# Performance work log

Measured on AMD Instinct MI355X. Metric: run time of the kernel, lower is better.

The kernel has to match this reference:

```python
import jax, jax.numpy as jnp
import numpy as np

B, T, NODES, DEG = 16, 50, 62, 8
IN, C, H, NC, K = 64, 128, 256, 3, 5
G = B * T            # num_graphs
N = G * NODES        # total nodes
E = G * NODES * DEG  # total edges (before self loops)


def setup_inputs() -> dict:
    key = jax.random.key(0)
    ks = jax.random.split(key, 12)
    # random within-graph edges, PyG-batched with node offsets
    rng = np.random.RandomState(0)
    src = rng.randint(0, NODES, size=(G, NODES * DEG))
    dst = rng.randint(0, NODES, size=(G, NODES * DEG))
    off = (np.arange(G) * NODES)[:, None]
    edge_index = jnp.asarray(np.stack([(src + off).ravel(), (dst + off).ravel()]), dtype=jnp.int32)

    def glorot(k, shape, fan_in):
        return jax.random.normal(k, shape, jnp.float32) / np.sqrt(fan_in)

    return {
        "x": jax.random.normal(ks[0], (N, IN), jnp.float32),
        "edge_index": edge_index,
        "edge_attr": jax.random.normal(ks[1], (E, 1), jnp.float32),
        "W_l": glorot(ks[2], (IN, C), IN), "b_l": jnp.zeros((C,), jnp.float32),
        "W_r": glorot(ks[3], (IN, C), IN), "b_r": jnp.zeros((C,), jnp.float32),
        "W_e": glorot(ks[4], (1, C), 1),
        "att": glorot(ks[5], (C,), C),
        "bias_out": jnp.zeros((C,), jnp.float32),
        "W_ih": glorot(ks[6], (3 * H, C), C), "W_hh": glorot(ks[7], (3 * H, H), H),
        "b_ih": jnp.zeros((3 * H,), jnp.float32), "b_hh": jnp.zeros((3 * H,), jnp.float32),
        "W1": glorot(ks[8], (H, H // 2), H), "b1": jnp.zeros((H // 2,), jnp.float32),
        "W2": glorot(ks[9], (H // 2, NC), H // 2), "b2": jnp.zeros((NC,), jnp.float32),
    }


def _forward(x, edge_index, edge_attr, W_l, b_l, W_r, b_r, W_e, att, bias_out,
             W_ih, W_hh, b_ih, b_hh, W1, b1, W2, b2):
    n = x.shape[0]
    src, dst = edge_index[0], edge_index[1]

    # --- GATv2Conv: add self loops with edge_attr fill_value='mean' (PyG default) ---
    sum_attr = jax.ops.segment_sum(edge_attr, dst, num_segments=n)
    cnt = jax.ops.segment_sum(jnp.ones_like(dst, jnp.float32), dst, num_segments=n)
    loop_attr = sum_attr / jnp.clip(cnt, 1.0)[:, None]
    ar = jnp.arange(n, dtype=src.dtype)
    src2 = jnp.concatenate([src, ar])
    dst2 = jnp.concatenate([dst, ar])
    ea = jnp.concatenate([edge_attr, loop_attr], axis=0)

    xl = x @ W_l + b_l          # source-side transform
    xr = x @ W_r + b_r          # target-side transform
    ee = ea @ W_e               # edge embedding (lin_edge, bias=False)

    m = xl[src2] + xr[dst2] + ee                # [E2, C]
    e = jax.nn.leaky_relu(m, 0.2) @ att         # [E2]
    # scatter-softmax over incoming edges per target node (self loops => no empty segs)
    emax = jax.ops.segment_max(e, dst2, num_segments=n)
    ez = jnp.exp(e - emax[dst2])
    den = jax.ops.segment_sum(ez, dst2, num_segments=n)
    alpha = ez / den[dst2]                      # [E2]
    h_sp = jax.ops.segment_sum(alpha[:, None] * xl[src2], dst2, num_segments=n) + bias_out

    # --- mean pool per graph (uniform graph size => reshape) ---
    g = h_sp.reshape(G, NODES, C).mean(axis=1).reshape(B, T, C)

    # --- GRU (PyTorch gate order r, z, n) ---
    def step(h, xt):
        gx = xt @ W_ih.T + b_ih
        gh = h @ W_hh.T + b_hh
        xr_, xz, xn = jnp.split(gx, 3, axis=-1)
        hr, hz, hn = jnp.split(gh, 3, axis=-1)
        r = jax.nn.sigmoid(xr_ + hr)
        z = jax.nn.sigmoid(xz + hz)
        nn_ = jnp.tanh(xn + r * hn)
        h2 = (1.0 - z) * nn_ + z * h
        return h2, h2

    h0 = jnp.zeros((B, H), g.dtype)
    _, hs = jax.lax.scan(step, h0, jnp.swapaxes(g, 0, 1))  # [T,B,H]
    gru_out = jnp.swapaxes(hs, 0, 1)                       # [B,T,H]

    # --- classifier (dropout inactive at eval) ---
    scores = jax.nn.relu(gru_out @ W1 + b1) @ W2 + b2      # [B,T,NC]

    # --- top-k over time per class, then mean over k ---
    vals, idx = jax.lax.top_k(jnp.swapaxes(scores, 1, 2), K)  # [B,NC,K]
    return vals.mean(axis=-1), jnp.swapaxes(idx, 1, 2)        # [B,NC], [B,K,NC]


def reference(x, edge_index, edge_attr, W_l, b_l, W_r, b_r, W_e, att, bias_out,
              W_ih, W_hh, b_ih, b_hh, W1, b1, W2, b2):
    return _forward(x, edge_index, edge_attr, W_l, b_l, W_r, b_r, W_e, att, bias_out,
                    W_ih, W_hh, b_ih, b_hh, W1, b1, W2, b2)
```

## Files before the change

kernel.cpp:

```cpp
#include <hip/hip_runtime.h>
#include <math.h>

#define NNODES 62
#define NDEG 8
#define NGRAPH 800
#define NB 16
#define NT 50
#define NIN 64
#define NCH 128
#define NH 256
#define NCLS 3
#define NTOPK 5
#define NSL 8
#define EPG (NNODES*NDEG)
#define E2G (EPG + NNODES)
#define NTOTAL (NGRAPH*NNODES)
#define ETOTAL (NGRAPH*EPG)

__launch_bounds__(256, 2)
__global__ void k_xrl(const float* __restrict__ x,
                      const float* __restrict__ W_r, const float* __restrict__ b_r,
                      const float* __restrict__ W_l, const float* __restrict__ b_l,
                      float* __restrict__ xr, float* __restrict__ xl) {
    __shared__ __align__(16) float x_s[64 * NIN];
    __shared__ __align__(16) float wr_s[NIN * NCH];
    __shared__ __align__(16) float wl_s[NIN * NCH];
    const int blk = blockIdx.x;
    const int tid = threadIdx.x;
    const int base_v = blk * 64;

    {
        const float4* src = reinterpret_cast<const float4*>(x + (size_t)base_v * NIN);
        float4* dst = reinterpret_cast<float4*>(x_s);
        for (int i = tid; i < 64 * NIN / 4; i += 256) dst[i] = src[i];
        const float4* sr = reinterpret_cast<const float4*>(W_r);
        const float4* sl = reinterpret_cast<const float4*>(W_l);
        float4* dr = reinterpret_cast<float4*>(wr_s);
        float4* dl = reinterpret_cast<float4*>(wl_s);
        for (int i = tid; i < NIN * NCH / 4; i += 256) { dr[i] = sr[i]; dl[i] = sl[i]; }
    }
    __syncthreads();

    const int c4 = (tid & 31) * 4;
    const int ng = tid >> 5;
    float4 aR[8], aL[8];
    float4 br4 = *reinterpret_cast<const float4*>(b_r + c4);
    float4 bl4 = *reinterpret_cast<const float4*>(b_l + c4);
    #pragma unroll
    for (int j = 0; j < 8; ++j) { aR[j] = br4; aL[j] = bl4; }

    const float* xs = x_s + (ng * 8) * NIN;
    for (int k4 = 0; k4 < NIN; k4 += 4) {
        float4 xv[8];
        #pragma unroll
        for (int j = 0; j < 8; ++j)
            xv[j] = *reinterpret_cast<const float4*>(&xs[j * NIN + k4]);
        #pragma unroll
        for (int kk = 0; kk < 4; ++kk) {
            float4 wr = *reinterpret_cast<const float4*>(&wr_s[(k4 + kk) * NCH + c4]);
            float4 wl = *reinterpret_cast<const float4*>(&wl_s[(k4 + kk) * NCH + c4]);
            #pragma unroll
            for (int j = 0; j < 8; ++j) {
                float xk = (kk == 0) ? xv[j].x : (kk == 1) ? xv[j].y
                         : (kk == 2) ? xv[j].z : xv[j].w;
                aR[j].x += xk * wr.x; aR[j].y += xk * wr.y;
                aR[j].z += xk * wr.z; aR[j].w += xk * wr.w;
                aL[j].x += xk * wl.x; aL[j].y += xk * wl.y;
                aL[j].z += xk * wl.z; aL[j].w += xk * wl.w;
            }
        }
    }
    #pragma unroll
    for (int j = 0; j < 8; ++j) {
        int v = base_v + ng * 8 + j;
        *reinterpret_cast<float4*>(xr + (size_t)v * NCH + c4) = aR[j];
        *reinterpret_cast<float4*>(xl + (size_t)v * NCH + c4) = aL[j];
    }
}

__global__ void k_transpose(const float* __restrict__ src, float* __restrict__ dst,
                            int rows, int cols) {
    int idx = blockIdx.x * blockDim.x + threadIdx.x;
    if (idx >= rows * cols) return;
    int r = idx / cols;
    int c = idx - r * cols;
    dst[c * rows + r] = src[idx];
}

__launch_bounds__(256, 4)
__global__ void k_gat(const int* __restrict__ ei, const float* __restrict__ eattr,
                      const float* __restrict__ W_e, const float* __restrict__ att,
                      const float* __restrict__ bias_out,
                      const float* __restrict__ xr_all, const float* __restrict__ xl_all,
                      float* __restrict__ g_all) {
    __shared__ __align__(16) float xl_s[NNODES * NCH];
    __shared__ unsigned short csr_src[E2G];
    __shared__ float csr_attr[E2G];
    __shared__ float csr_e[E2G];
    __shared__ unsigned short off_s[NNODES + 2];
    __shared__ unsigned cur_s[NNODES];
    __shared__ unsigned cnt_s[NNODES];
    __shared__ float asum_s[NNODES];
    __shared__ float la_s[NNODES];
    __shared__ float gacc_s[4 * NCH];

    const int g = blockIdx.x;
    const int tid = threadIdx.x;
    const int base_e = g * EPG;
    const int base_n = g * NNODES;

    for (int v = tid; v < NNODES; v += 256) { asum_s[v] = 0.f; cnt_s[v] = 0u; cur_s[v] = 0u; }
    {
        const float4* src = reinterpret_cast<const float4*>(xl_all + (size_t)base_n * NCH);
        float4* dst = reinterpret_cast<float4*>(xl_s);
        for (int i = tid; i < NNODES * NCH / 4; i += 256) dst[i] = src[i];
    }
    int s0 = -1, d0 = 0, s1 = -1, d1 = 0;
    float a0 = 0.f, a1 = 0.f;
    {
        int j0 = tid * 2, j1 = tid * 2 + 1;
        if (j0 < EPG) { s0 = ei[base_e + j0] - base_n; d0 = ei[ETOTAL + base_e + j0] - base_n; a0 = eattr[base_e + j0]; }
        if (j1 < EPG) { s1 = ei[base_e + j1] - base_n; d1 = ei[ETOTAL + base_e + j1] - base_n; a1 = eattr[base_e + j1]; }
    }
    __syncthreads();

    if (s0 >= 0) { atomicAdd(&cnt_s[d0], 1u); atomicAdd(&asum_s[d0], a0); }
    if (s1 >= 0) { atomicAdd(&cnt_s[d1], 1u); atomicAdd(&asum_s[d1], a1); }
    __syncthreads();

    if (tid < 64) {
        unsigned val = (tid < NNODES) ? (cnt_s[tid] + 1u) : 0u;
        unsigned xsc = val;
        #pragma unroll
        for (int dlt = 1; dlt < 64; dlt <<= 1) {
            unsigned o = __shfl_up(xsc, dlt, 64);
            if (tid >= dlt) xsc += o;
        }
        if (tid < NNODES) {
            off_s[tid] = (unsigned short)(xsc - val);
            la_s[tid] = asum_s[tid] / fmaxf((float)cnt_s[tid], 1.f);
        }
        if (tid == NNODES - 1) off_s[NNODES] = (unsigned short)xsc;
    }
    __syncthreads();

    if (s0 >= 0) { int sl = off_s[d0] + (int)atomicAdd(&cur_s[d0], 1u); csr_src[sl] = (unsigned short)s0; csr_attr[sl] = a0; }
    if (s1 >= 0) { int sl = off_s[d1] + (int)atomicAdd(&cur_s[d1], 1u); csr_src[sl] = (unsigned short)s1; csr_attr[sl] = a1; }
    if (tid < NNODES) { int sl = off_s[tid + 1] - 1; csr_src[sl] = (unsigned short)tid; csr_attr[sl] = la_s[tid]; }
    __syncthreads();

    const int wave = tid >> 6;
    const int lane = tid & 63;
    const int sub = lane & 15;
    const int gslot = wave * 4 + (lane >> 4);
    const int cb = sub * 8;

    float we0[8], at0[8];
    #pragma unroll
    for (int i = 0; i < 8; ++i) { we0[i] = W_e[cb + i]; at0[i] = att[cb + i]; }

    float acc[8];
    #pragma unroll
    for (int i = 0; i < 8; ++i) acc[i] = 0.f;

    for (int v = gslot; v < NNODES; v += 16) {
        const float* xrp = xr_all + (size_t)(base_n + v) * NCH + cb;
        float4 xr0 = *reinterpret_cast<const float4*>(xrp);
        float4 xr1 = *reinterpret_cast<const float4*>(xrp + 4);
        const int lo = off_s[v], hi = off_s[v + 1];
        float m = -INFINITY, ssum = 0.f;
        for (int sl = lo; sl < hi; ++sl) {
            int src = csr_src[sl];
            float a = csr_attr[sl];
            float4 x0 = *reinterpret_cast<const float4*>(&xl_s[src * NCH + cb]);
            float4 x1 = *reinterpret_cast<const float4*>(&xl_s[src * NCH + cb + 4]);
            float m0, t = 0.f;
            m0 = x0.x + xr0.x + a * we0[0]; t += (m0 >= 0.f ? m0 : 0.2f * m0) * at0[0];
            m0 = x0.y + xr0.y + a * we0[1]; t += (m0 >= 0.f ? m0 : 0.2f * m0) * at0[1];
            m0 = x0.z + xr0.z + a * we0[2]; t += (m0 >= 0.f ? m0 : 0.2f * m0) * at0[2];
            m0 = x0.w + xr0.w + a * we0[3]; t += (m0 >= 0.f ? m0 : 0.2f * m0) * at0[3];
            m0 = x1.x + xr1.x + a * we0[4]; t += (m0 >= 0.f ? m0 : 0.2f * m0) * at0[4];
            m0 = x1.y + xr1.y + a * we0[5]; t += (m0 >= 0.f ? m0 : 0.2f * m0) * at0[5];
            m0 = x1.z + xr1.z + a * we0[6]; t += (m0 >= 0.f ? m0 : 0.2f * m0) * at0[6];
            m0 = x1.w + xr1.w + a * we0[7]; t += (m0 >= 0.f ? m0 : 0.2f * m0) * at0[7];
            t += __shfl_xor(t, 1, 64);
            t += __shfl_xor(t, 2, 64);
            t += __shfl_xor(t, 4, 64);
            t += __shfl_xor(t, 8, 64);
            if (sub == 0) csr_e[sl] = t;
            float mn = fmaxf(m, t);
            ssum = ssum * __expf(m - mn) + __expf(t - mn);
            m = mn;
        }
        float inv = 1.f / ssum;
        for (int sl = lo; sl < hi; ++sl) {
            int src = csr_src[sl];
            float al = __expf(csr_e[sl] - m) * inv;
            float4 x0 = *reinterpret_cast<const float4*>(&xl_s[src * NCH + cb]);
            float4 x1 = *reinterpret_cast<const float4*>(&xl_s[src * NCH + cb + 4]);
            acc[0] += al * x0.x; acc[1] += al * x0.y;
            acc[2] += al * x0.z; acc[3] += al * x0.w;
            acc[4] += al * x1.x; acc[5] += al * x1.y;
            acc[6] += al * x1.z; acc[7] += al * x1.w;
        }
    }
    #pragma unroll
    for (int i = 0; i < 8; ++i) {
        acc[i] += __shfl_xor(acc[i], 16, 64);
        acc[i] += __shfl_xor(acc[i], 32, 64);
    }
    if ((lane >> 4) == 0) {
        *reinterpret_cast<float4*>(&gacc_s[wave * NCH + cb]) =
            make_float4(acc[0], acc[1], acc[2], acc[3]);
        *reinterpret_cast<float4*>(&gacc_s[wave * NCH + cb + 4]) =
            make_float4(acc[4], acc[5], acc[6], acc[7]);
    }
    __syncthreads();

    for (int c = tid; c < NCH; c += 256) {
        float v = (gacc_s[c] + gacc_s[NCH + c] + gacc_s[2 * NCH + c] + gacc_s[3 * NCH + c])
                      * (1.f / NNODES) + bias_out[c];
        g_all[(size_t)g * NCH + c] = v;
    }
}

__global__ void k_gx(const float* __restrict__ g_all, const float* __restrict__ W_ihT,
                     const float* __restrict__ b_ih, const float* __restrict__ b_hh,
                     float* __restrict__ gx_all, unsigned long long* __restrict__ h_pub) {
    if (blockIdx.x < 32)
        h_pub[(size_t)blockIdx.x * 256 + threadIdx.x] = 0ull;
    int idx = blockIdx.x * blockDim.x + threadIdx.x;
    if (idx >= NGRAPH * 3 * NH) return;
    int gi = idx / (3 * NH);
    int o = idx - gi * (3 * NH);
    float acc = b_ih[o] + (o < 2 * NH ? b_hh[o] : 0.f);
    const float* grow = g_all + (size_t)gi * NCH;
    for (int c = 0; c < NCH; ++c) acc += grow[c] * W_ihT[c * (3 * NH) + o];
    gx_all[idx] = acc;
}

__launch_bounds__(256)
__global__ void k_gru(const float* __restrict__ gx_all, const float* __restrict__ W_hh,
                      const float* __restrict__ b_hh, float* __restrict__ h_all,
                      unsigned long long* __restrict__ h_pub) {
    __shared__ __align__(16) float h_s[NH];
    __shared__ float gh_s[96];
    __shared__ float gx_s[2][96];

    const int bid = blockIdx.x;
    const int b = bid >> 3;
    const int s = bid & 7;
    const int tid = threadIdx.x;
    const int wv = tid >> 6;
    const int g = tid >> 1;
    const int l = tid & 1;

    float4 Wv[32];
    if (tid < 192) {
        int row = (g / 32) * NH + 32 * s + (g & 31);
        const float* wr = W_hh + (size_t)row * NH + 128 * l;
        #pragma unroll
        for (int j = 0; j < 32; ++j) Wv[j] = *reinterpret_cast<const float4*>(wr + 4 * j);
    }
    const float bhn = (tid < 32) ? b_hh[2 * NH + 32 * s + tid] : 0.f;
    const int own_lo = 32 * s, own_hi = own_lo + 32;

    for (int i = tid; i < NH; i += 256) h_s[i] = 0.f;
    if (wv == 3) {
        int i = tid - 192;
        int o = (i < 32) ? (32 * s + i) : (NH + 32 * s + (i - 32));
        gx_s[0][i] = gx_all[(size_t)(b * NT) * (3 * NH) + o];
        if (i < 32) gx_s[0][i + 64] = gx_all[(size_t)(b * NT) * (3 * NH) + 2 * NH + 32 * s + i];
    }
    __syncthreads();

    for (int t = 0; t < NT; ++t) {
        const int par = (t + 1) & 1;
        if (wv == 3) {
            int i = tid - 192;
            if (t + 1 < NT) {
                size_t base = (size_t)(b * NT + t + 1) * (3 * NH);
                int o = (i < 32) ? (32 * s + i) : (NH + 32 * s + (i - 32));
                gx_s[par][i] = gx_all[base + o];
                if (i < 32) gx_s[par][i + 64] = gx_all[base + 2 * NH + 32 * s + i];
            }
        } else {
            float a0 = 0.f, a1 = 0.f, a2 = 0.f, a3 = 0.f;
            #pragma unroll
            for (int j = 0; j < 32; ++j) {
                float4 hv = *reinterpret_cast<const float4*>(&h_s[128 * l + 4 * j]);
                float4 w = Wv[j];
                a0 += w.x * hv.x; a1 += w.y * hv.y; a2 += w.z * hv.z; a3 += w.w * hv.w;
            }
            float acc = (a0 + a1) + (a2 + a3);
            acc += __shfl_xor(acc, 1, 64);
            if (l == 0) gh_s[g] = acc;
        }
        __syncthreads();

        if (tid < 32) {
            const float* gx = gx_s[t & 1];
            float r = 1.f / (1.f + expf(-(gx[tid] + gh_s[tid])));
            float z = 1.f / (1.f + expf(-(gx[32 + tid] + gh_s[32 + tid])));
            float n = tanhf(gx[64 + tid] + r * (gh_s[64 + tid] + bhn));
            int o = own_lo + tid;
            float hv = (1.f - z) * n + z * h_s[o];
            h_all[(size_t)(b * NT + t) * NH + o] = hv;
            unsigned long long w = ((unsigned long long)(unsigned)(t + 1) << 32)
                                 | (unsigned long long)__float_as_uint(hv);
            __hip_atomic_store(&h_pub[((size_t)b * 2 + par) * NH + o], w,
                               __ATOMIC_RELAXED, __HIP_MEMORY_SCOPE_AGENT);
            h_s[o] = hv;
        }
        if (tid < own_lo || tid >= own_hi) {
            const unsigned long long* p = &h_pub[((size_t)b * 2 + par) * NH + tid];
            unsigned long long w;
            const unsigned target = (unsigned)(t + 1);
            while ((unsigned)((w = __hip_atomic_load(p, __ATOMIC_RELAXED,
                                                     __HIP_MEMORY_SCOPE_AGENT)) >> 32) != target)
                ;
            h_s[tid] = __uint_as_float((unsigned)w);
        }
        __syncthreads();
    }
}

__launch_bounds__(128)
__global__ void k_cls(const float* __restrict__ h_all,
                      const float* __restrict__ W1, const float* __restrict__ b1,
                      const float* __restrict__ W2, const float* __restrict__ b2,
                      float* __restrict__ sc_all) {
    __shared__ float h_s[NH];
    __shared__ float s1_s[NH / 2];
    const int bt = blockIdx.x;
    const int tid = threadIdx.x;
    h_s[tid] = h_all[(size_t)bt * NH + tid];
    h_s[tid + 128] = h_all[(size_t)bt * NH + tid + 128];
    __syncthreads();
    float acc = b1[tid];
    #pragma unroll 8
    for (int k = 0; k < NH; ++k) acc += h_s[k] * W1[k * (NH / 2) + tid];
    s1_s[tid] = fmaxf(acc, 0.f);
    __syncthreads();
    if (tid < NCLS) {
        float a = b2[tid];
        for (int k = 0; k < NH / 2; ++k) a += s1_s[k] * W2[k * NCLS + tid];
        sc_all[bt * NCLS + tid] = a;
    }
}

__global__ void k_topk(const float* __restrict__ sc_all, float* __restrict__ out) {
    int tid = threadIdx.x;
    if (tid >= NB * NCLS) return;
    int b = tid / NCLS;
    int c = tid - b * NCLS;
    float vals[NT];
    for (int t = 0; t < NT; ++t) vals[t] = sc_all[(b * NT + t) * NCLS + c];
    float sum = 0.f;
    for (int k = 0; k < NTOPK; ++k) {
        float best = -INFINITY; int bi = 0;
        for (int t = 0; t < NT; ++t) {
            if (vals[t] > best) { best = vals[t]; bi = t; }
        }
        vals[bi] = -INFINITY;
        sum += best;
        out[NB * NCLS + b * (NTOPK * NCLS) + k * NCLS + c] = (float)bi;
    }
    out[b * NCLS + c] = sum * (1.f / NTOPK);
}

extern "C" void kernel_launch(void* const* d_in, const int* in_sizes, int n_in,
                              void* d_out, int out_size, void* d_ws, size_t ws_size,
                              hipStream_t stream) {
    const float* x        = (const float*)d_in[0];
    const int*   ei       = (const int*)  d_in[1];
    const float* eattr    = (const float*)d_in[2];
    const float* W_l      = (const float*)d_in[3];
    const float* b_l      = (const float*)d_in[4];
    const float* W_r      = (const float*)d_in[5];
    const float* b_r      = (const float*)d_in[6];
    const float* W_e      = (const float*)d_in[7];
    const float* att      = (const float*)d_in[8];
    const float* bias_out = (const float*)d_in[9];
    const float* W_ih     = (const float*)d_in[10];
    const float* W_hh     = (const float*)d_in[11];
    const float* b_ih     = (const float*)d_in[12];
    const float* b_hh     = (const float*)d_in[13];
    const float* W1       = (const float*)d_in[14];
    const float* b1       = (const float*)d_in[15];
    const float* W2       = (const float*)d_in[16];
    const float* b2       = (const float*)d_in[17];
    float* out = (float*)d_out;

    float* ws = (float*)d_ws;
    float* xr_all = ws;
    float* xl_all = xr_all + (size_t)NTOTAL * NCH;
    float* g_all  = xl_all + (size_t)NTOTAL * NCH;
    float* gx_all = g_all + NGRAPH * NCH;
    float* W_ihT  = gx_all + NGRAPH * 3 * NH;
    float* h_all  = W_ihT + NCH * 3 * NH;
    float* sc_all = h_all + (size_t)NGRAPH * NH;
    unsigned long long* h_pub = (unsigned long long*)xr_all;

    k_xrl<<<NTOTAL / 64, 256, 0, stream>>>(x, W_r, b_r, W_l, b_l, xr_all, xl_all);
    k_transpose<<<(3 * NH * NCH + 255) / 256, 256, 0, stream>>>(W_ih, W_ihT, 3 * NH, NCH);
    k_gat<<<NGRAPH, 256, 0, stream>>>(ei, eattr, W_e, att, bias_out, xr_all, xl_all, g_all);
    k_gx<<<(NGRAPH * 3 * NH + 255) / 256, 256, 0, stream>>>(g_all, W_ihT, b_ih, b_hh, gx_all, h_pub);
    k_gru<<<NB * NSL, 256, 0, stream>>>(gx_all, W_hh, b_hh, h_all, h_pub);
    k_cls<<<NB * NT, 128, 0, stream>>>(h_all, W1, b1, W2, b2, sc_all);
    k_topk<<<1, 64, 0, stream>>>(sc_all, out);
}
```

Before: 227.4 us.

## Split GRU across 16 blocks per batch and fold W_ih transpose into projection kernel

```diff
diff --git a/kernel.cpp b/kernel.cpp
--- a/kernel.cpp
+++ b/kernel.cpp
@@ -11,22 +11,32 @@
 #define NH 256
 #define NCLS 3
 #define NTOPK 5
-#define NSL 8
+#define NSL 16
 #define EPG (NNODES*NDEG)
 #define E2G (EPG + NNODES)
 #define NTOTAL (NGRAPH*NNODES)
 #define ETOTAL (NGRAPH*EPG)
+#define NXB (NTOTAL/64)
+#define TTB 128
 
 __launch_bounds__(256, 2)
 __global__ void k_xrl(const float* __restrict__ x,
                       const float* __restrict__ W_r, const float* __restrict__ b_r,
                       const float* __restrict__ W_l, const float* __restrict__ b_l,
+                      const float* __restrict__ W_ih, float* __restrict__ W_ihT,
                       float* __restrict__ xr, float* __restrict__ xl) {
     __shared__ __align__(16) float x_s[64 * NIN];
     __shared__ __align__(16) float wr_s[NIN * NCH];
     __shared__ __align__(16) float wl_s[NIN * NCH];
     const int blk = blockIdx.x;
     const int tid = threadIdx.x;
+    if (blk >= NXB) {
+        for (int idx = (blk - NXB) * 256 + tid; idx < 3 * NH * NCH; idx += TTB * 256) {
+            int r = idx / NCH, c = idx - r * NCH;
+            W_ihT[c * (3 * NH) + r] = W_ih[idx];
+        }
+        return;
+    }
     const int base_v = blk * 64;
 
     {
@@ -78,15 +88,6 @@
     }
 }
 
-__global__ void k_transpose(const float* __restrict__ src, float* __restrict__ dst,
-                            int rows, int cols) {
-    int idx = blockIdx.x * blockDim.x + threadIdx.x;
-    if (idx >= rows * cols) return;
-    int r = idx / cols;
-    int c = idx - r * cols;
-    dst[c * rows + r] = src[idx];
-}
-
 __launch_bounds__(256, 4)
 __global__ void k_gat(const int* __restrict__ ei, const float* __restrict__ eattr,
                       const float* __restrict__ W_e, const float* __restrict__ att,
@@ -174,15 +175,15 @@
             float a = csr_attr[sl];
             float4 x0 = *reinterpret_cast<const float4*>(&xl_s[src * NCH + cb]);
             float4 x1 = *reinterpret_cast<const float4*>(&xl_s[src * NCH + cb + 4]);
-            float m0, t = 0.f;
-            m0 = x0.x + xr0.x + a * we0[0]; t += (m0 >= 0.f ? m0 : 0.2f * m0) * at0[0];
-            m0 = x0.y + xr0.y + a * we0[1]; t += (m0 >= 0.f ? m0 : 0.2f * m0) * at0[1];
-            m0 = x0.z + xr0.z + a * we0[2]; t += (m0 >= 0.f ? m0 : 0.2f * m0) * at0[2];
-            m0 = x0.w + xr0.w + a * we0[3]; t += (m0 >= 0.f ? m0 : 0.2f * m0) * at0[3];
-            m0 = x1.x + xr1.x + a * we0[4]; t += (m0 >= 0.f ? m0 : 0.2f * m0) * at0[4];
-            m0 = x1.y + xr1.y + a * we0[5]; t += (m0 >= 0.f ? m0 : 0.2f * m0) * at0[5];
-            m0 = x1.z + xr1.z + a * we0[6]; t += (m0 >= 0.f ? m0 : 0.2f * m0) * at0[6];
-            m0 = x1.w + xr1.w + a * we0[7]; t += (m0 >= 0.f ? m0 : 0.2f * m0) * at0[7];
+            float mi, t = 0.f;
+            mi = x0.x + xr0.x + a * we0[0]; t += (mi >= 0.f ? mi : 0.2f * mi) * at0[0];
+            mi = x0.y + xr0.y + a * we0[1]; t += (mi >= 0.f ? mi : 0.2f * mi) * at0[1];
+            mi = x0.z + xr0.z + a * we0[2]; t += (mi >= 0.f ? mi : 0.2f * mi) * at0[2];
+            mi = x0.w + xr0.w + a * we0[3]; t += (mi >= 0.f ? mi : 0.2f * mi) * at0[3];
+            mi = x1.x + xr1.x + a * we0[4]; t += (mi >= 0.f ? mi : 0.2f * mi) * at0[4];
+            mi = x1.y + xr1.y + a * we0[5]; t += (mi >= 0.f ? mi : 0.2f * mi) * at0[5];
+            mi = x1.z + xr1.z + a * we0[6]; t += (mi >= 0.f ? mi : 0.2f * mi) * at0[6];
+            mi = x1.w + xr1.w + a * we0[7]; t += (mi >= 0.f ? mi : 0.2f * mi) * at0[7];
             t += __shfl_xor(t, 1, 64);
             t += __shfl_xor(t, 2, 64);
             t += __shfl_xor(t, 4, 64);
@@ -239,70 +240,78 @@
     gx_all[idx] = acc;
 }
 
-__launch_bounds__(256)
+__launch_bounds__(256, 1)
 __global__ void k_gru(const float* __restrict__ gx_all, const float* __restrict__ W_hh,
                       const float* __restrict__ b_hh, float* __restrict__ h_all,
                       unsigned long long* __restrict__ h_pub) {
     __shared__ __align__(16) float h_s[NH];
-    __shared__ float gh_s[96];
-    __shared__ float gx_s[2][96];
+    __shared__ float gh_s[48];
+    __shared__ float gx_s[2][48];
 
     const int bid = blockIdx.x;
-    const int b = bid >> 3;
-    const int s = bid & 7;
+    const int b = bid >> 4;
+    const int s = bid & 15;
     const int tid = threadIdx.x;
     const int wv = tid >> 6;
-    const int g = tid >> 1;
-    const int l = tid & 1;
-
-    float4 Wv[32];
+    const int g = tid >> 2;
+    const int l = tid & 3;
+
+    float4 Wv[16];
     if (tid < 192) {
-        int row = (g / 32) * NH + 32 * s + (g & 31);
-        const float* wr = W_hh + (size_t)row * NH + 128 * l;
+        int row = (g < 16) ? (NSL * s + g)
+                : (g < 32) ? (NH + NSL * s + (g - 16))
+                           : (2 * NH + NSL * s + (g - 32));
+        const float* wr = W_hh + (size_t)row * NH + 64 * l;
         #pragma unroll
-        for (int j = 0; j < 32; ++j) Wv[j] = *reinterpret_cast<const float4*>(wr + 4 * j);
-    }
-    const float bhn = (tid < 32) ? b_hh[2 * NH + 32 * s + tid] : 0.f;
-    const int own_lo = 32 * s, own_hi = own_lo + 32;
+        for (int j = 0; j < 16; ++j) {
+            int jeff = (j + 2 * l) & 15;
+            Wv[j] = *reinterpret_cast<const float4*>(wr + 4 * jeff);
+        }
+    }
+    const float bhn = (tid < NSL) ? b_hh[2 * NH + NSL * s + tid] : 0.f;
+    const int own_lo = NSL * s, own_hi = NSL * s + NSL;
 
     for (int i = tid; i < NH; i += 256) h_s[i] = 0.f;
     if (wv == 3) {
         int i = tid - 192;
-        int o = (i < 32) ? (32 * s + i) : (NH + 32 * s + (i - 32));
-        gx_s[0][i] = gx_all[(size_t)(b * NT) * (3 * NH) + o];
-        if (i < 32) gx_s[0][i + 64] = gx_all[(size_t)(b * NT) * (3 * NH) + 2 * NH + 32 * s + i];
+        if (i < 48) {
+            int o = (i < 16) ? (NSL * s + i) : (i < 32) ? (NH + NSL * s + i - 16)
+                                                        : (2 * NH + NSL * s + i - 32);
+            gx_s[0][i] = gx_all[(size_t)(b * NT + 0) * (3 * NH) + o];
+        }
     }
     __syncthreads();
 
     for (int t = 0; t < NT; ++t) {
-        const int par = (t + 1) & 1;
         if (wv == 3) {
             int i = tid - 192;
-            if (t + 1 < NT) {
-                size_t base = (size_t)(b * NT + t + 1) * (3 * NH);
-                int o = (i < 32) ? (32 * s + i) : (NH + 32 * s + (i - 32));
-                gx_s[par][i] = gx_all[base + o];
-                if (i < 32) gx_s[par][i + 64] = gx_all[base + 2 * NH + 32 * s + i];
+            if (i < 48 && t + 1 < NT) {
+                int o = (i < 16) ? (NSL * s + i) : (i < 32) ? (NH + NSL * s + i - 16)
+                                                            : (2 * NH + NSL * s + i - 32);
+                gx_s[(t + 1) & 1][i] = gx_all[(size_t)(b * NT + t + 1) * (3 * NH) + o];
             }
         } else {
             float a0 = 0.f, a1 = 0.f, a2 = 0.f, a3 = 0.f;
             #pragma unroll
-            for (int j = 0; j < 32; ++j) {
-                float4 hv = *reinterpret_cast<const float4*>(&h_s[128 * l + 4 * j]);
+            for (int j = 0; j < 16; ++j) {
+                int jeff = (j + 2 * l) & 15;
+                float4 hv = *reinterpret_cast<const float4*>(&h_s[64 * l + 4 * jeff]);
                 float4 w = Wv[j];
                 a0 += w.x * hv.x; a1 += w.y * hv.y; a2 += w.z * hv.z; a3 += w.w * hv.w;
             }
             float acc = (a0 + a1) + (a2 + a3);
             acc += __shfl_xor(acc, 1, 64);
+            acc += __shfl_xor(acc, 2, 64);
             if (l == 0) gh_s[g] = acc;
         }
         __syncthreads();
 
-        if (tid < 32) {
+        const int par = (t + 1) & 1;
+        if (tid < NSL) {
             const float* gx = gx_s[t & 1];
             float r = 1.f / (1.f + expf(-(gx[tid] + gh_s[tid])));
-            float z = 1.f / (1.f + expf(-(gx[32 + tid] + gh_s[32 + tid])));
-            float n = tanhf(gx[64 + tid] + r * (gh_s[64 + tid] + bhn));
+            float z = 1.f / (1.f + expf(-(gx[16 + tid] + gh_s[16 + tid])));
+            float n = tanhf(gx[32 + tid] + r * (gh_s[32 + tid] + bhn));
             int o = own_lo + tid;
             float hv = (1.f - z) * n + z * h_s[o];
             h_all[(size_t)(b * NT + t) * NH + o] = hv;
@@ -318,7 +327,7 @@
             const unsigned target = (unsigned)(t + 1);
             while ((unsigned)((w = __hip_atomic_load(p, __ATOMIC_RELAXED,
                                                      __HIP_MEMORY_SCOPE_AGENT)) >> 32) != target)
-                ;
+                __builtin_amdgcn_s_sleep(1);
             h_s[tid] = __uint_as_float((unsigned)w);
         }
         __syncthreads();
@@ -402,10 +411,10 @@
     float* sc_all = h_all + (size_t)NGRAPH * NH;
     unsigned long long* h_pub = (unsigned long long*)xr_all;
 
-    k_xrl<<<NTOTAL / 64, 256, 0, stream>>>(x, W_r, b_r, W_l, b_l, xr_all, xl_all);
-    k_transpose<<<(3 * NH * NCH + 255) / 256, 256, 0, stream>>>(W_ih, W_ihT, 3 * NH, NCH);
+    k_xrl<<<NXB + TTB, 256, 0, stream>>>(x, W_r, b_r, W_l, b_l, W_ih, W_ihT, xr_all, xl_all);
     k_gat<<<NGRAPH, 256, 0, stream>>>(ei, eattr, W_e, att, bias_out, xr_all, xl_all, g_all);
-    k_gx<<<(NGRAPH * 3 * NH + 255) / 256, 256, 0, stream>>>(g_all, W_ihT, b_ih, b_hh, gx_all, h_pub);
+    k_gx<<<(NGRAPH * 3 * NH + 255) / 256, 256, 0, stream>>>(g_all, W_ihT, b_ih, b_hh,
+                                                            gx_all, h_pub);
     k_gru<<<NB * NSL, 256, 0, stream>>>(gx_all, W_hh, b_hh, h_all, h_pub);
     k_cls<<<NB * NT, 128, 0, stream>>>(h_all, W1, b1, W2, b2, sc_all);
     k_topk<<<1, 64, 0, stream>>>(sc_all, out);
```

Result: faster. 212.9 us (-6.4%).
